# Kernel tuning notes

Measured on AMD Instinct MI355X. Metric: run time of the kernel, lower is better.

Reference implementation:

```python
import jax, jax.numpy as jnp
import numpy as np

B, N = 8, 2048
IN_F, MID1, HID, MID2, OUT_F = 128, 128, 128, 128, 128
BIG = 9e15  # matches torch's 9000000000000000.0 additive mask constant


def _linear_params(key, out_d, in_d):
    # torch Linear layout: W is [out, in]
    kw, kb = jax.random.split(key)
    w = jax.random.normal(kw, (out_d, in_d), jnp.float32) * (1.0 / np.sqrt(in_d))
    b = jax.random.normal(kb, (out_d,), jnp.float32) * 0.01
    return w, b


def setup_inputs() -> dict:
    key = jax.random.key(0)
    ks = jax.random.split(key, 16)
    h = jax.random.normal(ks[0], (B, N, IN_F), jnp.float32)
    adj = jax.random.randint(ks[1], (B, N, N), 0, 2).astype(jnp.float32)
    vae2_fetures = jax.random.normal(ks[2], (B, N, OUT_F), jnp.float32)
    Wv1, bv1 = _linear_params(ks[3], MID1, IN_F)
    Wk1, bk1 = _linear_params(ks[4], MID1, IN_F)
    Wq1, bq1 = _linear_params(ks[5], MID1, IN_F)
    Wo1, bo1 = _linear_params(ks[6], HID, MID1)
    Wv2, bv2 = _linear_params(ks[7], MID2, HID)
    Wk2, bk2 = _linear_params(ks[8], MID2, HID)
    Wq2, bq2 = _linear_params(ks[9], MID2, HID)
    Wo2, bo2 = _linear_params(ks[10], OUT_F, MID2)
    Wf, bf = _linear_params(ks[11], OUT_F, 2 * OUT_F)
    return {
        "h": h, "adj": adj, "vae2_fetures": vae2_fetures,
        "Wv1": Wv1, "bv1": bv1, "Wk1": Wk1, "bk1": bk1, "Wq1": Wq1, "bq1": bq1,
        "Wo1": Wo1, "bo1": bo1,
        "Wv2": Wv2, "bv2": bv2, "Wk2": Wk2, "bk2": bk2, "Wq2": Wq2, "bq2": bq2,
        "Wo2": Wo2, "bo2": bo2, "Wf": Wf, "bf": bf,
    }


def _lin(x, W, b):
    return jnp.einsum('bnd,od->bno', x, W) + b


def _masked_att_block(x, adj, Wq, bq, Wk, bk, Wv, bv):
    v = jax.nn.relu(_lin(x, Wv, bv))          # [B,N,D]
    q = jax.nn.relu(_lin(x, Wq, bq))          # [B,N,D]
    k = jax.nn.relu(_lin(x, Wk, bk))          # [B,N,D]
    s = jnp.einsum('bnd,bmd->bnm', q, k)       # [B,N,N]
    masked = s * adj - BIG * (1.0 - adj)       # multiplicative + additive mask
    att = jax.nn.softmax(masked, axis=-1)
    return jnp.einsum('bnm,bmd->bnd', att, v)


def reference(h, adj, vae2_fetures,
              Wv1, bv1, Wk1, bk1, Wq1, bq1, Wo1, bo1,
              Wv2, bv2, Wk2, bk2, Wq2, bq2, Wo2, bo2,
              Wf, bf):
    f1 = _masked_att_block(h, adj, Wq1, bq1, Wk1, bk1, Wv1, bv1)
    f1 = _lin(f1, Wo1, bo1)                    # [B,N,HID]
    f2 = _masked_att_block(f1, adj, Wq2, bq2, Wk2, bk2, Wv2, bv2)
    f2 = _lin(f2, Wo2, bo2)                    # [B,N,OUT_F]
    f3 = jnp.concatenate([f2, vae2_fetures], axis=2)
    return _lin(f3, Wf, bf)                    # [B,N,OUT_F]
```

## Files before the change

kernel.cpp:

```cpp
#include <hip/hip_runtime.h>

typedef short s16x8 __attribute__((ext_vector_type(8)));
typedef float f32x4 __attribute__((ext_vector_type(4)));
typedef unsigned short u16x4v __attribute__((ext_vector_type(4)));

#define NSPLIT 4
#define NROWS 16384
#define MSHIFT 44.0f

__device__ __forceinline__ unsigned short f2bf(float f) {
  union { float fl; unsigned int i; } v; v.fl = f;
  unsigned int x = v.i;
  x += 0x7fffu + ((x >> 16) & 1u);
  return (unsigned short)(x >> 16);
}
__device__ __forceinline__ s16x8 load8_bf16(const unsigned short* p) {
  return *(const s16x8*)p;
}
__device__ __forceinline__ s16x8 load8_f32(const float* p) {
  float4 a = *(const float4*)p;
  float4 b = *(const float4*)(p + 4);
  s16x8 r;
  r[0] = (short)f2bf(a.x); r[1] = (short)f2bf(a.y);
  r[2] = (short)f2bf(a.z); r[3] = (short)f2bf(a.w);
  r[4] = (short)f2bf(b.x); r[5] = (short)f2bf(b.y);
  r[6] = (short)f2bf(b.z); r[7] = (short)f2bf(b.w);
  return r;
}

__global__ __launch_bounds__(256) void pack_kernel(
    const float4* __restrict__ adj4, unsigned long long* __restrict__ mask)
{
  const int lane = threadIdx.x & 63;
  const size_t nvec = (size_t)NROWS * 2048 / 4;
  const size_t stride = (size_t)gridDim.x * 256;
  for (size_t i = (size_t)blockIdx.x * 256 + threadIdx.x; i < nvec; i += stride) {
    float4 v = adj4[i];
    unsigned long long n = (v.x != 0.f ? 1u : 0u) | (v.y != 0.f ? 2u : 0u) |
                           (v.z != 0.f ? 4u : 0u) | (v.w != 0.f ? 8u : 0u);
    unsigned long long word = n << (4 * (lane & 15));
    word |= __shfl_xor(word, 1, 64);
    word |= __shfl_xor(word, 2, 64);
    word |= __shfl_xor(word, 4, 64);
    word |= __shfl_xor(word, 8, 64);
    if ((lane & 15) == 0) mask[(i * 4) >> 6] = word;
  }
}

template <int MODE>
__device__ __forceinline__ void qkv_body(
    const float* __restrict__ X, const float* __restrict__ W,
    const float* __restrict__ bias, unsigned short* __restrict__ out)
{
  const int t = threadIdx.x;
  const int w = t >> 6;
  const int lane = t & 63;
  const int l15 = lane & 15;
  const int quad = lane >> 4;
  const int mbase = blockIdx.x * 16;

  s16x8 a[4];
  const float* ar = X + (size_t)(mbase + l15) * 128;
#pragma unroll
  for (int ks = 0; ks < 4; ++ks) a[ks] = load8_f32(ar + ks * 32 + quad * 8);

#pragma unroll
  for (int nt = 0; nt < 2; ++nt) {
    const int n = (w * 2 + nt) * 16 + l15;
    f32x4 acc = {0.f, 0.f, 0.f, 0.f};
    const float* wr = W + (size_t)n * 128;
#pragma unroll
    for (int ks = 0; ks < 4; ++ks)
      acc = __builtin_amdgcn_mfma_f32_16x16x32_bf16(
          a[ks], load8_f32(wr + ks * 32 + quad * 8), acc, 0, 0, 0);
    const float bv = bias[n];
    if (MODE == 0) {
#pragma unroll
      for (int r = 0; r < 4; ++r)
        out[(size_t)(mbase + quad * 4 + r) * 128 + n] = f2bf(fmaxf(acc[r] + bv, 0.f));
    } else {
      const int b  = mbase >> 11;
      const int nn = (mbase & 2047) + quad * 4;
      u16x4v pk;
#pragma unroll
      for (int r = 0; r < 4; ++r) pk[r] = f2bf(fmaxf(acc[r] + bv, 0.f));
      *(u16x4v*)(out + (size_t)(b * 128 + n) * 2048 + nn) = pk;
    }
  }
}

__global__ __launch_bounds__(256) void qkv1_kernel(
    const float* __restrict__ x,
    const float* __restrict__ Wq, const float* __restrict__ bq, unsigned short* __restrict__ oq,
    const float* __restrict__ Wk, const float* __restrict__ bk, unsigned short* __restrict__ ok,
    const float* __restrict__ Wv, const float* __restrict__ bv, unsigned short* __restrict__ ovt)
{
  if (blockIdx.y == 0)      qkv_body<0>(x, Wq, bq, oq);
  else if (blockIdx.y == 1) qkv_body<0>(x, Wk, bk, ok);
  else                      qkv_body<1>(x, Wv, bv, ovt);
}

__global__ __launch_bounds__(256, 2) void attn_kernel(
    const unsigned short* __restrict__ Q,
    const unsigned short* __restrict__ K,
    const unsigned short* __restrict__ VT,
    const unsigned long long* __restrict__ MASK,
    float* __restrict__ pO, float* __restrict__ pl)
{
  __shared__ __align__(16) unsigned short kbuf[64][136];
  __shared__ __align__(16) unsigned short vbuf[128][72];
  __shared__ __align__(16) unsigned short pbuf[4][32][72];

  const int t = threadIdx.x;
  const int w = t >> 6;
  const int lane = t & 63;
  const int l15 = lane & 15;
  const int quad = lane >> 4;

  const int gq0 = blockIdx.x * 128;
  const int b   = gq0 >> 11;
  const int q0  = gq0 & 2047;
  const int wq0 = q0 + w * 32;
  const int kc0 = blockIdx.y * 512;

  const unsigned short* Kb  = K  + (size_t)(b * 2048) * 128;
  const unsigned short* VTb = VT + (size_t)(b * 128) * 2048;
  const unsigned long long* Mb = MASK + (size_t)b * 2048 * 32;

  s16x8 qf[2][4];
#pragma unroll
  for (int mt = 0; mt < 2; ++mt) {
    const unsigned short* qrow = Q + (size_t)(gq0 + w * 32 + mt * 16 + l15) * 128;
#pragma unroll
    for (int ks = 0; ks < 4; ++ks) qf[mt][ks] = load8_bf16(qrow + ks * 32 + quad * 8);
  }

  s16x8 ones;
#pragma unroll
  for (int i = 0; i < 8; ++i) ones[i] = (short)0x3F80;

  f32x4 accO[2][8];
  f32x4 accL[2];
#pragma unroll
  for (int mt = 0; mt < 2; ++mt) {
    accL[mt] = (f32x4){0.f, 0.f, 0.f, 0.f};
#pragma unroll
    for (int dt = 0; dt < 8; ++dt) accO[mt][dt] = (f32x4){0.f, 0.f, 0.f, 0.f};
  }

  s16x8 kr[4], vr[4];
#pragma unroll
  for (int i = 0; i < 4; ++i) {
    int slot = i * 256 + t;
    kr[i] = load8_bf16(Kb + (size_t)(kc0 + (slot >> 4)) * 128 + (slot & 15) * 8);
    vr[i] = load8_bf16(VTb + (size_t)(slot >> 3) * 2048 + kc0 + (slot & 7) * 8);
  }

  for (int kc = kc0; kc < kc0 + 512; kc += 64) {
    __syncthreads();
#pragma unroll
    for (int i = 0; i < 4; ++i) {
      int slot = i * 256 + t;
      *(s16x8*)&kbuf[slot >> 4][(slot & 15) * 8] = kr[i];
      *(s16x8*)&vbuf[slot >> 3][(slot & 7) * 8]  = vr[i];
    }
    __syncthreads();

    unsigned long long mw[2][4];
#pragma unroll
    for (int mt = 0; mt < 2; ++mt)
#pragma unroll
      for (int r = 0; r < 4; ++r)
        mw[mt][r] = Mb[(size_t)(wq0 + mt * 16 + quad * 4 + r) * 32 + (kc >> 6)];

    if (kc + 64 < kc0 + 512) {
#pragma unroll
      for (int i = 0; i < 4; ++i) {
        int slot = i * 256 + t;
        kr[i] = load8_bf16(Kb + (size_t)(kc + 64 + (slot >> 4)) * 128 + (slot & 15) * 8);
        vr[i] = load8_bf16(VTb + (size_t)(slot >> 3) * 2048 + (kc + 64) + (slot & 7) * 8);
      }
    }

    f32x4 sv[2][4];
#pragma unroll
    for (int nt = 0; nt < 4; ++nt) {
      sv[0][nt] = (f32x4){0.f, 0.f, 0.f, 0.f};
      sv[1][nt] = (f32x4){0.f, 0.f, 0.f, 0.f};
#pragma unroll
      for (int ks = 0; ks < 4; ++ks) {
        s16x8 kf = *(const s16x8*)&kbuf[nt * 16 + l15][ks * 32 + quad * 8];
        sv[0][nt] = __builtin_amdgcn_mfma_f32_16x16x32_bf16(qf[0][ks], kf, sv[0][nt], 0, 0, 0);
        sv[1][nt] = __builtin_amdgcn_mfma_f32_16x16x32_bf16(qf[1][ks], kf, sv[1][nt], 0, 0, 0);
      }
    }

#pragma unroll
    for (int mt = 0; mt < 2; ++mt)
#pragma unroll
      for (int nt = 0; nt < 4; ++nt)
#pragma unroll
        for (int r = 0; r < 4; ++r) {
          float p = __expf(sv[mt][nt][r] - MSHIFT);
          p = ((mw[mt][r] >> (nt * 16 + l15)) & 1ull) ? p : 0.f;
          pbuf[w][mt * 16 + quad * 4 + r][nt * 16 + l15] = f2bf(p);
        }

    s16x8 pf[2][2];
#pragma unroll
    for (int mt = 0; mt < 2; ++mt)
#pragma unroll
      for (int ks = 0; ks < 2; ++ks)
        pf[mt][ks] = *(const s16x8*)&pbuf[w][mt * 16 + l15][ks * 32 + quad * 8];

#pragma unroll
    for (int mt = 0; mt < 2; ++mt)
#pragma unroll
      for (int ks = 0; ks < 2; ++ks)
        accL[mt] = __builtin_amdgcn_mfma_f32_16x16x32_bf16(ones, pf[mt][ks], accL[mt], 0, 0, 0);

#pragma unroll
    for (int dt = 0; dt < 8; ++dt) {
#pragma unroll
      for (int ks = 0; ks < 2; ++ks) {
        s16x8 vf = *(const s16x8*)&vbuf[dt * 16 + l15][ks * 32 + quad * 8];
        accO[0][dt] = __builtin_amdgcn_mfma_f32_16x16x32_bf16(vf, pf[0][ks], accO[0][dt], 0, 0, 0);
        accO[1][dt] = __builtin_amdgcn_mfma_f32_16x16x32_bf16(vf, pf[1][ks], accO[1][dt], 0, 0, 0);
      }
    }
  }

  float* pOs = pO + (size_t)blockIdx.y * NROWS * 128;
#pragma unroll
  for (int mt = 0; mt < 2; ++mt) {
    const int qg = gq0 + w * 32 + mt * 16 + l15;
#pragma unroll
    for (int dt = 0; dt < 8; ++dt)
      *(f32x4*)(pOs + (size_t)qg * 128 + dt * 16 + quad * 4) = accO[mt][dt];
  }
  if (quad == 0) {
#pragma unroll
    for (int mt = 0; mt < 2; ++mt)
      pl[blockIdx.y * NROWS + gq0 + w * 32 + mt * 16 + l15] = accL[mt][0];
  }
}

__device__ __forceinline__ void combine_splits(
    const float* __restrict__ pO, const float* __restrict__ pl, int grow0,
    unsigned short (*At)[136])
{
  const int t = threadIdx.x;
  const int row = t >> 4;
  const int col8 = (t & 15) * 8;
  const int grow = grow0 + row;
  float lsum = 0.f;
#pragma unroll
  for (int s = 0; s < NSPLIT; ++s) lsum += pl[s * NROWS + grow];
  const float inv = (lsum > 0.f) ? 1.f / lsum : 0.f;
  float acc8[8];
#pragma unroll
  for (int i = 0; i < 8; ++i) acc8[i] = 0.f;
#pragma unroll
  for (int s = 0; s < NSPLIT; ++s) {
    const float* p = pO + (size_t)s * NROWS * 128 + (size_t)grow * 128 + col8;
    float4 x0 = *(const float4*)p;
    float4 x1 = *(const float4*)(p + 4);
    acc8[0] += x0.x; acc8[1] += x0.y; acc8[2] += x0.z; acc8[3] += x0.w;
    acc8[4] += x1.x; acc8[5] += x1.y; acc8[6] += x1.z; acc8[7] += x1.w;
  }
#pragma unroll
  for (int i = 0; i < 8; ++i) At[row][col8 + i] = f2bf(acc8[i] * inv);
}

__global__ __launch_bounds__(256) void redqkv_kernel(
    const float* __restrict__ pO, const float* __restrict__ pl,
    const float* __restrict__ Wo, const float* __restrict__ bo,
    const float* __restrict__ Wq, const float* __restrict__ bq, unsigned short* __restrict__ oq,
    const float* __restrict__ Wk, const float* __restrict__ bk, unsigned short* __restrict__ ok,
    const float* __restrict__ Wv, const float* __restrict__ bv, unsigned short* __restrict__ ovt)
{
  __shared__ __align__(16) unsigned short At[16][136];
  __shared__ __align__(16) unsigned short Bt[16][136];
  const int t = threadIdx.x;
  const int grow0 = blockIdx.x * 16;

  combine_splits(pO, pl, grow0, At);
  __syncthreads();

  const int w = t >> 6;
  const int lane = t & 63;
  const int l15 = lane & 15;
  const int quad = lane >> 4;

  s16x8 a[4];
#pragma unroll
  for (int ks = 0; ks < 4; ++ks) a[ks] = *(const s16x8*)&At[l15][ks * 32 + quad * 8];
#pragma unroll
  for (int nt = 0; nt < 2; ++nt) {
    const int n = (w * 2 + nt) * 16 + l15;
    f32x4 acc = {0.f, 0.f, 0.f, 0.f};
    const float* wr = Wo + (size_t)n * 128;
#pragma unroll
    for (int ks = 0; ks < 4; ++ks)
      acc = __builtin_amdgcn_mfma_f32_16x16x32_bf16(
          a[ks], load8_f32(wr + ks * 32 + quad * 8), acc, 0, 0, 0);
    const float bv_ = bo[n];
#pragma unroll
    for (int r = 0; r < 4; ++r) Bt[quad * 4 + r][n] = f2bf(acc[r] + bv_);
  }
  __syncthreads();

  s16x8 a2[4];
#pragma unroll
  for (int ks = 0; ks < 4; ++ks) a2[ks] = *(const s16x8*)&Bt[l15][ks * 32 + quad * 8];

#pragma unroll
  for (int which = 0; which < 3; ++which) {
    const float* W = (which == 0) ? Wq : (which == 1) ? Wk : Wv;
    const float* bb = (which == 0) ? bq : (which == 1) ? bk : bv;
    unsigned short* out = (which == 0) ? oq : (which == 1) ? ok : ovt;
#pragma unroll
    for (int nt = 0; nt < 2; ++nt) {
      const int n = (w * 2 + nt) * 16 + l15;
      f32x4 acc = {0.f, 0.f, 0.f, 0.f};
      const float* wr = W + (size_t)n * 128;
#pragma unroll
      for (int ks = 0; ks < 4; ++ks)
        acc = __builtin_amdgcn_mfma_f32_16x16x32_bf16(
            a2[ks], load8_f32(wr + ks * 32 + quad * 8), acc, 0, 0, 0);
      const float bv_ = bb[n];
      if (which < 2) {
#pragma unroll
        for (int r = 0; r < 4; ++r)
          out[(size_t)(grow0 + quad * 4 + r) * 128 + n] = f2bf(fmaxf(acc[r] + bv_, 0.f));
      } else {
        const int b  = grow0 >> 11;
        const int nn = (grow0 & 2047) + quad * 4;
        u16x4v pk;
#pragma unroll
        for (int r = 0; r < 4; ++r) pk[r] = f2bf(fmaxf(acc[r] + bv_, 0.f));
        *(u16x4v*)(out + (size_t)(b * 128 + n) * 2048 + nn) = pk;
      }
    }
  }
}

__global__ __launch_bounds__(256) void redfinal_kernel(
    const float* __restrict__ pO, const float* __restrict__ pl,
    const float* __restrict__ Wo, const float* __restrict__ bo,
    const float* __restrict__ Wf, const float* __restrict__ bff,
    const float* __restrict__ vae2, float* __restrict__ out)
{
  __shared__ __align__(16) unsigned short At[16][136];
  __shared__ __align__(16) unsigned short Bt[16][136];
  const int t = threadIdx.x;
  const int grow0 = blockIdx.x * 16;

  combine_splits(pO, pl, grow0, At);
  __syncthreads();

  const int w = t >> 6;
  const int lane = t & 63;
  const int l15 = lane & 15;
  const int quad = lane >> 4;

  s16x8 a[4];
#pragma unroll
  for (int ks = 0; ks < 4; ++ks) a[ks] = *(const s16x8*)&At[l15][ks * 32 + quad * 8];
#pragma unroll
  for (int nt = 0; nt < 2; ++nt) {
    const int n = (w * 2 + nt) * 16 + l15;
    f32x4 acc = {0.f, 0.f, 0.f, 0.f};
    const float* wr = Wo + (size_t)n * 128;
#pragma unroll
    for (int ks = 0; ks < 4; ++ks)
      acc = __builtin_amdgcn_mfma_f32_16x16x32_bf16(
          a[ks], load8_f32(wr + ks * 32 + quad * 8), acc, 0, 0, 0);
    const float bv_ = bo[n];
#pragma unroll
    for (int r = 0; r < 4; ++r) Bt[quad * 4 + r][n] = f2bf(acc[r] + bv_);
  }
  __syncthreads();

  s16x8 a1[4], a2[4];
#pragma unroll
  for (int ks = 0; ks < 4; ++ks) a1[ks] = *(const s16x8*)&Bt[l15][ks * 32 + quad * 8];
  const float* vrow = vae2 + (size_t)(grow0 + l15) * 128;
#pragma unroll
  for (int ks = 0; ks < 4; ++ks) a2[ks] = load8_f32(vrow + ks * 32 + quad * 8);
#pragma unroll
  for (int nt = 0; nt < 2; ++nt) {
    const int n = (w * 2 + nt) * 16 + l15;
    f32x4 acc = {0.f, 0.f, 0.f, 0.f};
    const float* wr = Wf + (size_t)n * 256;
#pragma unroll
    for (int ks = 0; ks < 4; ++ks)
      acc = __builtin_amdgcn_mfma_f32_16x16x32_bf16(
          a1[ks], load8_f32(wr + ks * 32 + quad * 8), acc, 0, 0, 0);
#pragma unroll
    for (int ks = 0; ks < 4; ++ks)
      acc = __builtin_amdgcn_mfma_f32_16x16x32_bf16(
          a2[ks], load8_f32(wr + 128 + ks * 32 + quad * 8), acc, 0, 0, 0);
    const float bv_ = bff[n];
#pragma unroll
    for (int r = 0; r < 4; ++r)
      out[(size_t)(grow0 + quad * 4 + r) * 128 + n] = acc[r] + bv_;
  }
}

extern "C" void kernel_launch(void* const* d_in, const int* in_sizes, int n_in,
                              void* d_out, int out_size, void* d_ws, size_t ws_size,
                              hipStream_t stream)
{
  const float* h    = (const float*)d_in[0];
  const float* adj  = (const float*)d_in[1];
  const float* vae2 = (const float*)d_in[2];
  const float* Wv1  = (const float*)d_in[3];
  const float* bv1  = (const float*)d_in[4];
  const float* Wk1  = (const float*)d_in[5];
  const float* bk1  = (const float*)d_in[6];
  const float* Wq1  = (const float*)d_in[7];
  const float* bq1  = (const float*)d_in[8];
  const float* Wo1  = (const float*)d_in[9];
  const float* bo1  = (const float*)d_in[10];
  const float* Wv2  = (const float*)d_in[11];
  const float* bv2  = (const float*)d_in[12];
  const float* Wk2  = (const float*)d_in[13];
  const float* bk2  = (const float*)d_in[14];
  const float* Wq2  = (const float*)d_in[15];
  const float* bq2  = (const float*)d_in[16];
  const float* Wo2  = (const float*)d_in[17];
  const float* bo2  = (const float*)d_in[18];
  const float* Wf   = (const float*)d_in[19];
  const float* bff  = (const float*)d_in[20];

  char* wsb = (char*)d_ws;
  const size_t MB = 1u << 20;
  unsigned short* s_q  = (unsigned short*)(wsb + 0 * MB);
  unsigned short* s_k  = (unsigned short*)(wsb + 4 * MB);
  unsigned short* s_vt = (unsigned short*)(wsb + 8 * MB);
  unsigned long long* maskp = (unsigned long long*)(wsb + 12 * MB);
  float* pO = (float*)(wsb + 16 * MB);
  float* pl = (float*)(wsb + 48 * MB);

  pack_kernel<<<dim3(4096), dim3(256), 0, stream>>>((const float4*)adj, maskp);
  qkv1_kernel<<<dim3(1024, 3), dim3(256), 0, stream>>>(
      h, Wq1, bq1, s_q, Wk1, bk1, s_k, Wv1, bv1, s_vt);
  attn_kernel<<<dim3(128, NSPLIT), dim3(256), 0, stream>>>(
      s_q, s_k, s_vt, maskp, pO, pl);
  redqkv_kernel<<<dim3(1024), dim3(256), 0, stream>>>(
      pO, pl, Wo1, bo1, Wq2, bq2, s_q, Wk2, bk2, s_k, Wv2, bv2, s_vt);
  attn_kernel<<<dim3(128, NSPLIT), dim3(256), 0, stream>>>(
      s_q, s_k, s_vt, maskp, pO, pl);
  redfinal_kernel<<<dim3(1024), dim3(256), 0, stream>>>(
      pO, pl, Wo2, bo2, Wf, bff, vae2, (float*)d_out);
}
```

Baseline: 401.1 us.

## Drop LDS staging in attention, keep P in registers via permuted V layout

The attention kernel no longer stages K, V and P through shared memory. K and V fragments are read straight from global memory, and the S MFMA is transposed so each lane holds the P values it needs. V^T is written with a column permutation so those register-resident P fragments line up with the V fragments without an LDS round trip. The split-K count is doubled, occupancy is raised to 3 blocks per CU, and the pl buffer is moved to fit the larger partial-output workspace. The trade is more global/L2 traffic for K and V, and more split partials to combine, in exchange for removing the barriers and LDS transfers.

```diff
diff --git a/kernel.cpp b/kernel.cpp
--- a/kernel.cpp
+++ b/kernel.cpp
@@ -4,7 +4,7 @@
 typedef float f32x4 __attribute__((ext_vector_type(4)));
 typedef unsigned short u16x4v __attribute__((ext_vector_type(4)));
 
-#define NSPLIT 4
+#define NSPLIT 8
 #define NROWS 16384
 #define MSHIFT 44.0f
 
@@ -26,6 +26,9 @@
   r[4] = (short)f2bf(b.x); r[5] = (short)f2bf(b.y);
   r[6] = (short)f2bf(b.z); r[7] = (short)f2bf(b.w);
   return r;
+}
+__device__ __forceinline__ int vperm(int nn) {
+  return (nn & ~31) | (((nn >> 2) & 3) << 3) | (((nn >> 4) & 1) << 2);
 }
 
 __global__ __launch_bounds__(256) void pack_kernel(
@@ -84,7 +87,7 @@
       u16x4v pk;
 #pragma unroll
       for (int r = 0; r < 4; ++r) pk[r] = f2bf(fmaxf(acc[r] + bv, 0.f));
-      *(u16x4v*)(out + (size_t)(b * 128 + n) * 2048 + nn) = pk;
+      *(u16x4v*)(out + (size_t)(b * 128 + n) * 2048 + vperm(nn)) = pk;
     }
   }
 }
@@ -100,17 +103,13 @@
   else                      qkv_body<1>(x, Wv, bv, ovt);
 }
 
-__global__ __launch_bounds__(256, 2) void attn_kernel(
+__global__ __launch_bounds__(256, 3) void attn_kernel(
     const unsigned short* __restrict__ Q,
     const unsigned short* __restrict__ K,
     const unsigned short* __restrict__ VT,
     const unsigned long long* __restrict__ MASK,
     float* __restrict__ pO, float* __restrict__ pl)
 {
-  __shared__ __align__(16) unsigned short kbuf[64][136];
-  __shared__ __align__(16) unsigned short vbuf[128][72];
-  __shared__ __align__(16) unsigned short pbuf[4][32][72];
-
   const int t = threadIdx.x;
   const int w = t >> 6;
   const int lane = t & 63;
@@ -121,7 +120,7 @@
   const int b   = gq0 >> 11;
   const int q0  = gq0 & 2047;
   const int wq0 = q0 + w * 32;
-  const int kc0 = blockIdx.y * 512;
+  const int kc0 = blockIdx.y * (2048 / NSPLIT);
 
   const unsigned short* Kb  = K  + (size_t)(b * 2048) * 128;
   const unsigned short* VTb = VT + (size_t)(b * 128) * 2048;
@@ -148,70 +147,50 @@
     for (int dt = 0; dt < 8; ++dt) accO[mt][dt] = (f32x4){0.f, 0.f, 0.f, 0.f};
   }
 
-  s16x8 kr[4], vr[4];
-#pragma unroll
-  for (int i = 0; i < 4; ++i) {
-    int slot = i * 256 + t;
-    kr[i] = load8_bf16(Kb + (size_t)(kc0 + (slot >> 4)) * 128 + (slot & 15) * 8);
-    vr[i] = load8_bf16(VTb + (size_t)(slot >> 3) * 2048 + kc0 + (slot & 7) * 8);
-  }
-
-  for (int kc = kc0; kc < kc0 + 512; kc += 64) {
-    __syncthreads();
-#pragma unroll
-    for (int i = 0; i < 4; ++i) {
-      int slot = i * 256 + t;
-      *(s16x8*)&kbuf[slot >> 4][(slot & 15) * 8] = kr[i];
-      *(s16x8*)&vbuf[slot >> 3][(slot & 7) * 8]  = vr[i];
-    }
-    __syncthreads();
-
-    unsigned long long mw[2][4];
+  for (int kc = kc0; kc < kc0 + 2048 / NSPLIT; kc += 64) {
+    unsigned long long mw[2];
 #pragma unroll
     for (int mt = 0; mt < 2; ++mt)
-#pragma unroll
-      for (int r = 0; r < 4; ++r)
-        mw[mt][r] = Mb[(size_t)(wq0 + mt * 16 + quad * 4 + r) * 32 + (kc >> 6)];
-
-    if (kc + 64 < kc0 + 512) {
-#pragma unroll
-      for (int i = 0; i < 4; ++i) {
-        int slot = i * 256 + t;
-        kr[i] = load8_bf16(Kb + (size_t)(kc + 64 + (slot >> 4)) * 128 + (slot & 15) * 8);
-        vr[i] = load8_bf16(VTb + (size_t)(slot >> 3) * 2048 + (kc + 64) + (slot & 7) * 8);
-      }
-    }
+      mw[mt] = Mb[(size_t)(wq0 + mt * 16 + l15) * 32 + (kc >> 6)];
 
     f32x4 sv[2][4];
 #pragma unroll
     for (int nt = 0; nt < 4; ++nt) {
       sv[0][nt] = (f32x4){0.f, 0.f, 0.f, 0.f};
       sv[1][nt] = (f32x4){0.f, 0.f, 0.f, 0.f};
+      const unsigned short* krow = Kb + (size_t)(kc + nt * 16 + l15) * 128;
 #pragma unroll
       for (int ks = 0; ks < 4; ++ks) {
-        s16x8 kf = *(const s16x8*)&kbuf[nt * 16 + l15][ks * 32 + quad * 8];
-        sv[0][nt] = __builtin_amdgcn_mfma_f32_16x16x32_bf16(qf[0][ks], kf, sv[0][nt], 0, 0, 0);
-        sv[1][nt] = __builtin_amdgcn_mfma_f32_16x16x32_bf16(qf[1][ks], kf, sv[1][nt], 0, 0, 0);
+        s16x8 kf = load8_bf16(krow + ks * 32 + quad * 8);
+        sv[0][nt] = __builtin_amdgcn_mfma_f32_16x16x32_bf16(kf, qf[0][ks], sv[0][nt], 0, 0, 0);
+        sv[1][nt] = __builtin_amdgcn_mfma_f32_16x16x32_bf16(kf, qf[1][ks], sv[1][nt], 0, 0, 0);
       }
     }
 
+    float p[2][4][4];
 #pragma unroll
     for (int mt = 0; mt < 2; ++mt)
 #pragma unroll
       for (int nt = 0; nt < 4; ++nt)
 #pragma unroll
         for (int r = 0; r < 4; ++r) {
-          float p = __expf(sv[mt][nt][r] - MSHIFT);
-          p = ((mw[mt][r] >> (nt * 16 + l15)) & 1ull) ? p : 0.f;
-          pbuf[w][mt * 16 + quad * 4 + r][nt * 16 + l15] = f2bf(p);
+          float e = __expf(sv[mt][nt][r] - MSHIFT);
+          p[mt][nt][r] = ((mw[mt] >> (nt * 16 + quad * 4 + r)) & 1ull) ? e : 0.f;
         }
 
     s16x8 pf[2][2];
 #pragma unroll
     for (int mt = 0; mt < 2; ++mt)
 #pragma unroll
-      for (int ks = 0; ks < 2; ++ks)
-        pf[mt][ks] = *(const s16x8*)&pbuf[w][mt * 16 + l15][ks * 32 + quad * 8];
+      for (int ks = 0; ks < 2; ++ks) {
+        s16x8 v;
+#pragma unroll
+        for (int j = 0; j < 4; ++j) {
+          v[j]     = (short)f2bf(p[mt][2 * ks][j]);
+          v[j + 4] = (short)f2bf(p[mt][2 * ks + 1][j]);
+        }
+        pf[mt][ks] = v;
+      }
 
 #pragma unroll
     for (int mt = 0; mt < 2; ++mt)
@@ -221,9 +200,10 @@
 
 #pragma unroll
     for (int dt = 0; dt < 8; ++dt) {
+      const unsigned short* vrow = VTb + (size_t)(dt * 16 + l15) * 2048 + kc;
 #pragma unroll
       for (int ks = 0; ks < 2; ++ks) {
-        s16x8 vf = *(const s16x8*)&vbuf[dt * 16 + l15][ks * 32 + quad * 8];
+        s16x8 vf = load8_bf16(vrow + ks * 32 + quad * 8);
         accO[0][dt] = __builtin_amdgcn_mfma_f32_16x16x32_bf16(vf, pf[0][ks], accO[0][dt], 0, 0, 0);
         accO[1][dt] = __builtin_amdgcn_mfma_f32_16x16x32_bf16(vf, pf[1][ks], accO[1][dt], 0, 0, 0);
       }
@@ -339,7 +319,7 @@
         u16x4v pk;
 #pragma unroll
         for (int r = 0; r < 4; ++r) pk[r] = f2bf(fmaxf(acc[r] + bv_, 0.f));
-        *(u16x4v*)(out + (size_t)(b * 128 + n) * 2048 + nn) = pk;
+        *(u16x4v*)(out + (size_t)(b * 128 + n) * 2048 + vperm(nn)) = pk;
       }
     }
   }
@@ -441,7 +421,7 @@
   unsigned short* s_vt = (unsigned short*)(wsb + 8 * MB);
   unsigned long long* maskp = (unsigned long long*)(wsb + 12 * MB);
   float* pO = (float*)(wsb + 16 * MB);
-  float* pl = (float*)(wsb + 48 * MB);
+  float* pl = (float*)(wsb + 80 * MB);
 
   pack_kernel<<<dim3(4096), dim3(256), 0, stream>>>((const float4*)adj, maskp);
   qkv1_kernel<<<dim3(1024, 3), dim3(256), 0, stream>>>(
```

Result: slower. 595.6 us (+48.5%).
